# Kernel optimization log

Measured on AMD Instinct MI355X. Metric: run time of the kernel, lower is better.

Reference implementation:

```python
import jax, jax.numpy as jnp
import numpy as np

N = 50000
E = 1600000
D = 128
NUM_BOND_FEATS = 3
BOND_VOCAB = 5
BN_EPS = 1e-5


def setup_inputs() -> dict:
    key = jax.random.key(0)
    ks = jax.random.split(key, 12)
    x = jax.random.normal(ks[0], (N, D), dtype=jnp.float32)
    edge_attr = jax.random.randint(ks[1], (E, NUM_BOND_FEATS), 0, BOND_VOCAB, dtype=jnp.int64)
    src = jax.random.randint(ks[2], (E,), 0, N, dtype=jnp.int64)
    dst = jax.random.randint(ks[3], (E,), 0, N, dtype=jnp.int64)
    # BondEncoder: one embedding table per bond feature
    bond_emb = jax.random.normal(ks[4], (NUM_BOND_FEATS, BOND_VOCAB, D), dtype=jnp.float32) * 0.02
    # GIN eps parameter (init 0)
    eps = jnp.zeros((), dtype=jnp.float32)
    # MLP: Linear(D,D) -> BatchNorm1d(D) -> ReLU -> Linear(D,D)
    s = 1.0 / np.sqrt(D)
    W1 = jax.random.uniform(ks[5], (D, D), minval=-s, maxval=s, dtype=jnp.float32)
    b1 = jax.random.uniform(ks[6], (D,), minval=-s, maxval=s, dtype=jnp.float32)
    gamma = jnp.ones((D,), dtype=jnp.float32)
    beta = jnp.zeros((D,), dtype=jnp.float32)
    W2 = jax.random.uniform(ks[7], (D, D), minval=-s, maxval=s, dtype=jnp.float32)
    b2 = jax.random.uniform(ks[8], (D,), minval=-s, maxval=s, dtype=jnp.float32)
    return {"x": x, "edge_attr": edge_attr, "src": src, "dst": dst,
            "bond_emb": bond_emb, "eps": eps, "W1": W1, "b1": b1,
            "gamma": gamma, "beta": beta, "W2": W2, "b2": b2}


def reference(x, edge_attr, src, dst, bond_emb, eps, W1, b1, gamma, beta, W2, b2):
    # BondEncoder: sum of per-feature categorical embeddings -> [E, D]
    edge_embedding = bond_emb[jnp.arange(NUM_BOND_FEATS)[None, :], edge_attr].sum(axis=1)
    # copy_u gather + add edge emb + ReLU (per-edge messages)
    m = jax.nn.relu(x[src] + edge_embedding)            # [E, D]
    # scatter-sum aggregation to destination nodes
    agg = jax.ops.segment_sum(m, dst, num_segments=N)   # [N, D]
    h = (1.0 + eps) * x + agg
    # MLP: Linear -> BatchNorm (batch stats, training mode) -> ReLU -> Linear
    h1 = h @ W1 + b1
    mean = jnp.mean(h1, axis=0)
    var = jnp.var(h1, axis=0)
    hn = (h1 - mean) * jax.lax.rsqrt(var + BN_EPS) * gamma + beta
    out = jax.nn.relu(hn) @ W2 + b2
    return out
```

## Files before the change

### kernel.cpp

```cpp
#include <hip/hip_runtime.h>
#include <hip/hip_bf16.h>

#define NN 50000
#define NE 1600000
#define D 128
#define NB 196
#define CAP 9216
#define EPT 16

__device__ __forceinline__ void fma4(float4& acc, float s, const float4& w) {
  acc.x = fmaf(s, w.x, acc.x);
  acc.y = fmaf(s, w.y, acc.y);
  acc.z = fmaf(s, w.z, acc.z);
  acc.w = fmaf(s, w.w, acc.w);
}

__device__ __forceinline__ unsigned short f2bf(float f) {
  unsigned u = __float_as_uint(f);
  u += 0x7FFFu + ((u >> 16) & 1u);
  return (unsigned short)(u >> 16);
}
__device__ __forceinline__ float bf2f(unsigned short h) {
  return __uint_as_float((unsigned)h << 16);
}

__global__ __launch_bounds__(256) void k_half(const float* __restrict__ x,
                                              const float* __restrict__ bemb,
                                              ushort* __restrict__ xh,
                                              float* __restrict__ ctab) {
  const int gid = blockIdx.x * 256 + threadIdx.x;

  if (gid < 125 * D) {
    const int c = gid >> 7;
    const int k = gid & 127;
    ctab[gid] = bemb[(c / 25) * D + k] + bemb[(5 + (c % 25) / 5) * D + k] +
                bemb[(10 + c % 5) * D + k];
  }

  const int i4 = gid * 4;
  if (i4 < NN * D) {
    const float4 v = *(const float4*)(x + i4);
    ushort4 h;
    h.x = f2bf(v.x); h.y = f2bf(v.y); h.z = f2bf(v.z); h.w = f2bf(v.w);
    *(ushort4*)(xh + i4) = h;
  }
}

__global__ __launch_bounds__(256) void k_bin(const int* __restrict__ dst,
                                             const int* __restrict__ src,
                                             const int* __restrict__ ea,
                                             int* __restrict__ bucketCnt,
                                             unsigned* __restrict__ staging) {
  __shared__ int lcnt[NB], gbase[NB], lcur[NB];
  const int tid = threadIdx.x;
  for (int i = tid; i < NB; i += 256) { lcnt[i] = 0; lcur[i] = 0; }
  __syncthreads();

  const int gid = blockIdx.x * 256 + tid;
  const int e0 = gid * EPT;
  const bool act = (e0 < NE);

  int d[EPT];
  unsigned rec[EPT];
  if (act) {
    const int4* dp = (const int4*)(dst + e0);
    const int4* sp = (const int4*)(src + e0);
    const int4* ap = (const int4*)(ea + 3 * e0);
    int a[3 * EPT];
#pragma unroll
    for (int q = 0; q < (3 * EPT) / 4; ++q) {
      const int4 v = ap[q];
      a[4 * q + 0] = v.x; a[4 * q + 1] = v.y; a[4 * q + 2] = v.z; a[4 * q + 3] = v.w;
    }
#pragma unroll
    for (int q = 0; q < EPT / 4; ++q) {
      const int4 dv = dp[q];
      const int4 sv = sp[q];
      d[4 * q + 0] = dv.x; d[4 * q + 1] = dv.y; d[4 * q + 2] = dv.z; d[4 * q + 3] = dv.w;
      rec[4 * q + 0] = sv.x; rec[4 * q + 1] = sv.y; rec[4 * q + 2] = sv.z; rec[4 * q + 3] = sv.w;
    }
#pragma unroll
    for (int q = 0; q < EPT; ++q) {
      const unsigned cb = (unsigned)((a[3 * q] * 5 + a[3 * q + 1]) * 5 + a[3 * q + 2]);
      rec[q] |= (cb << 16) | ((unsigned)(d[q] & 255) << 23);
      atomicAdd(&lcnt[d[q] >> 8], 1);
    }
  }
  __syncthreads();
  for (int i = tid; i < NB; i += 256)
    gbase[i] = atomicAdd(&bucketCnt[i], lcnt[i]);
  __syncthreads();
  if (act) {
#pragma unroll
    for (int q = 0; q < EPT; ++q) {
      const int b = d[q] >> 8;
      const int r = atomicAdd(&lcur[b], 1) + gbase[b];
      if (r < CAP) staging[(size_t)b * CAP + r] = rec[q];
    }
  }
}

__global__ __launch_bounds__(256) void k_fine(const int* __restrict__ bucketCnt,
                                              const unsigned* __restrict__ staging,
                                              unsigned* __restrict__ packed2,
                                              int* __restrict__ beg,
                                              int* __restrict__ end) {
  __shared__ unsigned srec[CAP];
  __shared__ int hist[256], off[256], cur[256];
  const int tid = threadIdx.x;
  const int b = blockIdx.x;
  const int base = b * CAP;
  const int cnt = min(bucketCnt[b], CAP);

  hist[tid] = 0; cur[tid] = 0;
  for (int i = tid; i < cnt; i += 256) srec[i] = staging[base + i];
  __syncthreads();
  for (int i = tid; i < cnt; i += 256) atomicAdd(&hist[srec[i] >> 23], 1);
  __syncthreads();
  int v = hist[tid];
  off[tid] = v;
  __syncthreads();
  for (int s = 1; s < 256; s <<= 1) {
    const int u = (tid >= s) ? off[tid - s] : 0;
    __syncthreads();
    off[tid] += u;
    __syncthreads();
  }
  const int ex = off[tid] - v;
  __syncthreads();
  off[tid] = ex;
  __syncthreads();

  const int n = b * 256 + tid;
  if (n < NN) {
    beg[n] = base + off[tid];
    end[n] = base + off[tid] + hist[tid];
  }
  for (int i = tid; i < cnt; i += 256) {
    const unsigned u = srec[i];
    const int node = u >> 23;
    const int r = atomicAdd(&cur[node], 1);
    packed2[base + off[node] + r] = u & 0x7FFFFFu;
  }
}

__global__ __launch_bounds__(256, 4) void k_agg(const float* __restrict__ x,
                                                const ushort* __restrict__ xh,
                                                const float* __restrict__ ctab,
                                                const float* __restrict__ epsp,
                                                const int* __restrict__ beg,
                                                const int* __restrict__ end,
                                                const unsigned* __restrict__ packed2,
                                                float* __restrict__ hbuf) {
  const int lane = threadIdx.x & 31;
  const int n = blockIdx.x * 8 + (threadIdx.x >> 5);
  const int col = lane << 2;

  const int jb = beg[n];
  const int je = end[n];
  float4 acc = make_float4(0.f, 0.f, 0.f, 0.f);

  for (int j0 = jb; j0 < je; j0 += 32) {
    const int rem = min(32, je - j0);
    const int pk = (j0 + lane < je) ? (int)packed2[j0 + lane] : 0;
    int t = 0;
    for (; t + 8 <= rem; t += 8) {
      unsigned p[8];
#pragma unroll
      for (int i = 0; i < 8; ++i) p[i] = (unsigned)__shfl(pk, t + i, 32);
      ushort4 xs[8];
#pragma unroll
      for (int i = 0; i < 8; ++i)
        xs[i] = *(const ushort4*)(xh + (size_t)(p[i] & 0xFFFF) * D + col);
#pragma unroll
      for (int i = 0; i < 8; ++i) {
        const float4 ev = *(const float4*)(ctab + ((p[i] >> 16) & 0x7F) * D + col);
        acc.x += fmaxf(bf2f(xs[i].x) + ev.x, 0.f);
        acc.y += fmaxf(bf2f(xs[i].y) + ev.y, 0.f);
        acc.z += fmaxf(bf2f(xs[i].z) + ev.z, 0.f);
        acc.w += fmaxf(bf2f(xs[i].w) + ev.w, 0.f);
      }
    }
    for (; t < rem; ++t) {
      const unsigned p = (unsigned)__shfl(pk, t, 32);
      const ushort4 xv = *(const ushort4*)(xh + (size_t)(p & 0xFFFF) * D + col);
      const float4 ev = *(const float4*)(ctab + ((p >> 16) & 0x7F) * D + col);
      acc.x += fmaxf(bf2f(xv.x) + ev.x, 0.f);
      acc.y += fmaxf(bf2f(xv.y) + ev.y, 0.f);
      acc.z += fmaxf(bf2f(xv.z) + ev.z, 0.f);
      acc.w += fmaxf(bf2f(xv.w) + ev.w, 0.f);
    }
  }

  const float eps1 = 1.0f + epsp[0];
  const float4 xv = *(const float4*)(x + (size_t)n * D + col);
  acc.x += eps1 * xv.x;
  acc.y += eps1 * xv.y;
  acc.z += eps1 * xv.z;
  acc.w += eps1 * xv.w;
  *(float4*)(hbuf + (size_t)n * D + col) = acc;
}

__global__ __launch_bounds__(256, 2) void k_gemm1(const float* __restrict__ hbuf,
                                                  const float* __restrict__ W1,
                                                  const float* __restrict__ b1,
                                                  float* __restrict__ h1,
                                                  float* __restrict__ gsum,
                                                  float* __restrict__ gsumsq) {
  __shared__ float shT[64 * 64];
  __shared__ float sW[64 * 128];

  const int tid = threadIdx.x;
  const int row0 = blockIdx.x * 64;
  const int cg = tid & 31;
  const int rt = tid >> 5;
  const int cbase = cg * 4;
  const int rbase = rt * 8;

  float4 acc[8];
  const float4 bias = *(const float4*)(b1 + cbase);
#pragma unroll
  for (int r = 0; r < 8; ++r) acc[r] = bias;

  for (int kh = 0; kh < 2; ++kh) {
    __syncthreads();
    for (int i = tid; i < 1024; i += 256) {
      const int r = i & 63;
      const int kc = (i >> 6) << 2;
      const int gr = row0 + r;
      float4 v = make_float4(0.f, 0.f, 0.f, 0.f);
      if (gr < NN) v = *(const float4*)(hbuf + (size_t)gr * D + kh * 64 + kc);
      shT[(kc + 0) * 64 + r] = v.x;
      shT[(kc + 1) * 64 + r] = v.y;
      shT[(kc + 2) * 64 + r] = v.z;
      shT[(kc + 3) * 64 + r] = v.w;
    }
    for (int i = tid; i < 2048; i += 256) {
      const int k = i >> 5;
      const int c4 = (i & 31) << 2;
      *(float4*)(sW + k * 128 + c4) = *(const float4*)(W1 + (size_t)(kh * 64 + k) * D + c4);
    }
    __syncthreads();
    for (int k = 0; k < 64; ++k) {
      const float4 a_lo = *(const float4*)(shT + k * 64 + rbase);
      const float4 a_hi = *(const float4*)(shT + k * 64 + rbase + 4);
      const float4 w = *(const float4*)(sW + k * 128 + cbase);
      fma4(acc[0], a_lo.x, w); fma4(acc[1], a_lo.y, w);
      fma4(acc[2], a_lo.z, w); fma4(acc[3], a_lo.w, w);
      fma4(acc[4], a_hi.x, w); fma4(acc[5], a_hi.y, w);
      fma4(acc[6], a_hi.z, w); fma4(acc[7], a_hi.w, w);
    }
  }

  float4 cs = make_float4(0.f, 0.f, 0.f, 0.f);
  float4 cq = make_float4(0.f, 0.f, 0.f, 0.f);
#pragma unroll
  for (int r = 0; r < 8; ++r) {
    const int gr = row0 + rbase + r;
    if (gr < NN) {
      *(float4*)(h1 + (size_t)gr * D + cbase) = acc[r];
      cs.x += acc[r].x; cs.y += acc[r].y; cs.z += acc[r].z; cs.w += acc[r].w;
      cq.x += acc[r].x * acc[r].x; cq.y += acc[r].y * acc[r].y;
      cq.z += acc[r].z * acc[r].z; cq.w += acc[r].w * acc[r].w;
    }
  }
  __syncthreads();
  float* ssum = shT;
  float* ssq = shT + 128;
  if (tid < 128) { ssum[tid] = 0.f; ssq[tid] = 0.f; }
  __syncthreads();
  atomicAdd(&ssum[cbase + 0], cs.x);
  atomicAdd(&ssum[cbase + 1], cs.y);
  atomicAdd(&ssum[cbase + 2], cs.z);
  atomicAdd(&ssum[cbase + 3], cs.w);
  atomicAdd(&ssq[cbase + 0], cq.x);
  atomicAdd(&ssq[cbase + 1], cq.y);
  atomicAdd(&ssq[cbase + 2], cq.z);
  atomicAdd(&ssq[cbase + 3], cq.w);
  __syncthreads();
  if (tid < 128) {
    atomicAdd(&gsum[tid], ssum[tid]);
    atomicAdd(&gsumsq[tid], ssq[tid]);
  }
}

__global__ __launch_bounds__(256, 2) void k_gemm2(const float* __restrict__ hbuf,
                                                  const float* __restrict__ gsum,
                                                  const float* __restrict__ gsq,
                                                  const float* __restrict__ gamma,
                                                  const float* __restrict__ beta,
                                                  const float* __restrict__ W2,
                                                  const float* __restrict__ b2,
                                                  float* __restrict__ out) {
  __shared__ float shT[64 * 64];
  __shared__ float sW[64 * 128];

  const int tid = threadIdx.x;
  const int row0 = blockIdx.x * 64;
  const int cg = tid & 31;
  const int rt = tid >> 5;
  const int cbase = cg * 4;
  const int rbase = rt * 8;
  const float invN = 1.0f / (float)NN;

  float4 acc[8];
  const float4 bias = *(const float4*)(b2 + cbase);
#pragma unroll
  for (int r = 0; r < 8; ++r) acc[r] = bias;

  for (int kh = 0; kh < 2; ++kh) {
    __syncthreads();
    for (int i = tid; i < 1024; i += 256) {
      const int r = i & 63;
      const int kc = (i >> 6) << 2;
      const int gr = row0 + r;
      const int kk = kh * 64 + kc;
      const float4 gs = *(const float4*)(gsum + kk);
      const float4 gq = *(const float4*)(gsq + kk);
      const float4 gm = *(const float4*)(gamma + kk);
      const float4 bt = *(const float4*)(beta + kk);
      const float m0 = gs.x * invN, m1 = gs.y * invN, m2 = gs.z * invN, m3 = gs.w * invN;
      const float A0 = gm.x * rsqrtf(gq.x * invN - m0 * m0 + 1e-5f);
      const float A1 = gm.y * rsqrtf(gq.y * invN - m1 * m1 + 1e-5f);
      const float A2 = gm.z * rsqrtf(gq.z * invN - m2 * m2 + 1e-5f);
      const float A3 = gm.w * rsqrtf(gq.w * invN - m3 * m3 + 1e-5f);
      float4 v = make_float4(0.f, 0.f, 0.f, 0.f);
      if (gr < NN) {
        const float4 h = *(const float4*)(hbuf + (size_t)gr * D + kk);
        v.x = fmaxf(fmaf(h.x - m0, A0, bt.x), 0.f);
        v.y = fmaxf(fmaf(h.y - m1, A1, bt.y), 0.f);
        v.z = fmaxf(fmaf(h.z - m2, A2, bt.z), 0.f);
        v.w = fmaxf(fmaf(h.w - m3, A3, bt.w), 0.f);
      }
      shT[(kc + 0) * 64 + r] = v.x;
      shT[(kc + 1) * 64 + r] = v.y;
      shT[(kc + 2) * 64 + r] = v.z;
      shT[(kc + 3) * 64 + r] = v.w;
    }
    for (int i = tid; i < 2048; i += 256) {
      const int k = i >> 5;
      const int c4 = (i & 31) << 2;
      *(float4*)(sW + k * 128 + c4) = *(const float4*)(W2 + (size_t)(kh * 64 + k) * D + c4);
    }
    __syncthreads();
    for (int k = 0; k < 64; ++k) {
      const float4 a_lo = *(const float4*)(shT + k * 64 + rbase);
      const float4 a_hi = *(const float4*)(shT + k * 64 + rbase + 4);
      const float4 w = *(const float4*)(sW + k * 128 + cbase);
      fma4(acc[0], a_lo.x, w); fma4(acc[1], a_lo.y, w);
      fma4(acc[2], a_lo.z, w); fma4(acc[3], a_lo.w, w);
      fma4(acc[4], a_hi.x, w); fma4(acc[5], a_hi.y, w);
      fma4(acc[6], a_hi.z, w); fma4(acc[7], a_hi.w, w);
    }
  }

#pragma unroll
  for (int r = 0; r < 8; ++r) {
    const int gr = row0 + rbase + r;
    if (gr < NN) *(float4*)(out + (size_t)gr * D + cbase) = acc[r];
  }
}

extern "C" void kernel_launch(void* const* d_in, const int* in_sizes, int n_in,
                              void* d_out, int out_size, void* d_ws, size_t ws_size,
                              hipStream_t stream) {
  const float* x    = (const float*)d_in[0];
  const int* ea     = (const int*)d_in[1];
  const int* src    = (const int*)d_in[2];
  const int* dst    = (const int*)d_in[3];
  const float* bemb = (const float*)d_in[4];
  const float* epsp = (const float*)d_in[5];
  const float* W1   = (const float*)d_in[6];
  const float* b1   = (const float*)d_in[7];
  const float* gam  = (const float*)d_in[8];
  const float* bet  = (const float*)d_in[9];
  const float* W2   = (const float*)d_in[10];
  const float* b2   = (const float*)d_in[11];
  float* out = (float*)d_out;

  float* ws         = (float*)d_ws;
  float* hbuf       = ws;
  int* bucketCnt    = (int*)(ws + (size_t)NN * D);
  float* gsum       = ws + (size_t)NN * D + NB;
  float* gsumsq     = gsum + D;
  int* beg          = (int*)(gsumsq + D);
  int* endp         = beg + NN;
  float* ctab       = (float*)(endp + NN);
  ushort* xh        = (ushort*)(ctab + 125 * D);
  unsigned* staging = (unsigned*)(xh + (size_t)NN * D);
  unsigned* packed2 = staging + (size_t)NB * CAP;

  hipMemsetAsync(bucketCnt, 0, (size_t)(NB + 2 * D) * sizeof(int), stream);

  k_half<<<(NN * D / 4 + 255) / 256, 256, 0, stream>>>(x, bemb, xh, ctab);
  k_bin<<<(NE / EPT + 255) / 256, 256, 0, stream>>>(dst, src, ea, bucketCnt, staging);
  k_fine<<<NB, 256, 0, stream>>>(bucketCnt, staging, packed2, beg, endp);
  k_agg<<<NN / 8, 256, 0, stream>>>(x, xh, ctab, epsp, beg, endp, packed2, hbuf);
  k_gemm1<<<(NN + 63) / 64, 256, 0, stream>>>(hbuf, W1, b1, hbuf, gsum, gsumsq);
  k_gemm2<<<(NN + 63) / 64, 256, 0, stream>>>(hbuf, gsum, gsumsq, gam, bet, W2, b2, out);
}
```

Baseline: 319.6 us.

## Store edge-embedding table in bf16, widen agg loads, enlarge binning blocks

The combined bond embedding table is now stored as bf16, and the aggregation kernel switches to 16 lanes per node, each loading 8 columns with 16-byte loads. This halves table traffic and doubles the bytes per gather instruction. Separately, the binning and fine-sort kernels move to 1024-thread blocks, with binning doing 4 edges per thread instead of 16, and the agg occupancy hint rises to 6. Rounding the embedding table to bf16 adds some precision loss.

```diff
diff --git a/kernel.cpp b/kernel.cpp
--- a/kernel.cpp
+++ b/kernel.cpp
@@ -6,7 +6,7 @@
 #define D 128
 #define NB 196
 #define CAP 9216
-#define EPT 16
+#define EPT 4
 
 __device__ __forceinline__ void fma4(float4& acc, float s, const float4& w) {
   acc.x = fmaf(s, w.x, acc.x);
@@ -20,21 +20,33 @@
   u += 0x7FFFu + ((u >> 16) & 1u);
   return (unsigned short)(u >> 16);
 }
-__device__ __forceinline__ float bf2f(unsigned short h) {
-  return __uint_as_float((unsigned)h << 16);
+
+__device__ __forceinline__ void acc8(float* acc, const uint4& xv, const uint4& ev) {
+  const unsigned xx[4] = {xv.x, xv.y, xv.z, xv.w};
+  const unsigned ee[4] = {ev.x, ev.y, ev.z, ev.w};
+#pragma unroll
+  for (int q = 0; q < 4; ++q) {
+    const float xl = __uint_as_float(xx[q] << 16);
+    const float xh_ = __uint_as_float(xx[q] & 0xFFFF0000u);
+    const float el = __uint_as_float(ee[q] << 16);
+    const float eh = __uint_as_float(ee[q] & 0xFFFF0000u);
+    acc[2 * q + 0] += fmaxf(xl + el, 0.f);
+    acc[2 * q + 1] += fmaxf(xh_ + eh, 0.f);
+  }
 }
 
 __global__ __launch_bounds__(256) void k_half(const float* __restrict__ x,
                                               const float* __restrict__ bemb,
                                               ushort* __restrict__ xh,
-                                              float* __restrict__ ctab) {
+                                              ushort* __restrict__ cth) {
   const int gid = blockIdx.x * 256 + threadIdx.x;
 
   if (gid < 125 * D) {
     const int c = gid >> 7;
     const int k = gid & 127;
-    ctab[gid] = bemb[(c / 25) * D + k] + bemb[(5 + (c % 25) / 5) * D + k] +
-                bemb[(10 + c % 5) * D + k];
+    const float v = bemb[(c / 25) * D + k] + bemb[(5 + (c % 25) / 5) * D + k] +
+                    bemb[(10 + c % 5) * D + k];
+    cth[gid] = f2bf(v);
   }
 
   const int i4 = gid * 4;
@@ -46,39 +58,34 @@
   }
 }
 
-__global__ __launch_bounds__(256) void k_bin(const int* __restrict__ dst,
-                                             const int* __restrict__ src,
-                                             const int* __restrict__ ea,
-                                             int* __restrict__ bucketCnt,
-                                             unsigned* __restrict__ staging) {
+__global__ __launch_bounds__(1024) void k_bin(const int* __restrict__ dst,
+                                              const int* __restrict__ src,
+                                              const int* __restrict__ ea,
+                                              int* __restrict__ bucketCnt,
+                                              unsigned* __restrict__ staging) {
   __shared__ int lcnt[NB], gbase[NB], lcur[NB];
   const int tid = threadIdx.x;
-  for (int i = tid; i < NB; i += 256) { lcnt[i] = 0; lcur[i] = 0; }
-  __syncthreads();
-
-  const int gid = blockIdx.x * 256 + tid;
+  for (int i = tid; i < NB; i += 1024) { lcnt[i] = 0; lcur[i] = 0; }
+  __syncthreads();
+
+  const int gid = blockIdx.x * 1024 + tid;
   const int e0 = gid * EPT;
   const bool act = (e0 < NE);
 
   int d[EPT];
   unsigned rec[EPT];
   if (act) {
-    const int4* dp = (const int4*)(dst + e0);
-    const int4* sp = (const int4*)(src + e0);
+    const int4 dv = *(const int4*)(dst + e0);
+    const int4 sv = *(const int4*)(src + e0);
     const int4* ap = (const int4*)(ea + 3 * e0);
-    int a[3 * EPT];
-#pragma unroll
-    for (int q = 0; q < (3 * EPT) / 4; ++q) {
+    int a[12];
+#pragma unroll
+    for (int q = 0; q < 3; ++q) {
       const int4 v = ap[q];
       a[4 * q + 0] = v.x; a[4 * q + 1] = v.y; a[4 * q + 2] = v.z; a[4 * q + 3] = v.w;
     }
-#pragma unroll
-    for (int q = 0; q < EPT / 4; ++q) {
-      const int4 dv = dp[q];
-      const int4 sv = sp[q];
-      d[4 * q + 0] = dv.x; d[4 * q + 1] = dv.y; d[4 * q + 2] = dv.z; d[4 * q + 3] = dv.w;
-      rec[4 * q + 0] = sv.x; rec[4 * q + 1] = sv.y; rec[4 * q + 2] = sv.z; rec[4 * q + 3] = sv.w;
-    }
+    d[0] = dv.x; d[1] = dv.y; d[2] = dv.z; d[3] = dv.w;
+    rec[0] = sv.x; rec[1] = sv.y; rec[2] = sv.z; rec[3] = sv.w;
 #pragma unroll
     for (int q = 0; q < EPT; ++q) {
       const unsigned cb = (unsigned)((a[3 * q] * 5 + a[3 * q + 1]) * 5 + a[3 * q + 2]);
@@ -87,7 +94,7 @@
     }
   }
   __syncthreads();
-  for (int i = tid; i < NB; i += 256)
+  for (int i = tid; i < NB; i += 1024)
     gbase[i] = atomicAdd(&bucketCnt[i], lcnt[i]);
   __syncthreads();
   if (act) {
@@ -100,11 +107,11 @@
   }
 }
 
-__global__ __launch_bounds__(256) void k_fine(const int* __restrict__ bucketCnt,
-                                              const unsigned* __restrict__ staging,
-                                              unsigned* __restrict__ packed2,
-                                              int* __restrict__ beg,
-                                              int* __restrict__ end) {
+__global__ __launch_bounds__(1024) void k_fine(const int* __restrict__ bucketCnt,
+                                               const unsigned* __restrict__ staging,
+                                               unsigned* __restrict__ packed2,
+                                               int* __restrict__ beg,
+                                               int* __restrict__ end) {
   __shared__ unsigned srec[CAP];
   __shared__ int hist[256], off[256], cur[256];
   const int tid = threadIdx.x;
@@ -112,31 +119,32 @@
   const int base = b * CAP;
   const int cnt = min(bucketCnt[b], CAP);
 
-  hist[tid] = 0; cur[tid] = 0;
-  for (int i = tid; i < cnt; i += 256) srec[i] = staging[base + i];
-  __syncthreads();
-  for (int i = tid; i < cnt; i += 256) atomicAdd(&hist[srec[i] >> 23], 1);
-  __syncthreads();
-  int v = hist[tid];
-  off[tid] = v;
+  if (tid < 256) { hist[tid] = 0; cur[tid] = 0; }
+  for (int i = tid; i < cnt; i += 1024) srec[i] = staging[base + i];
+  __syncthreads();
+  for (int i = tid; i < cnt; i += 1024) atomicAdd(&hist[srec[i] >> 23], 1);
+  __syncthreads();
+  int v = 0;
+  if (tid < 256) { v = hist[tid]; off[tid] = v; }
   __syncthreads();
   for (int s = 1; s < 256; s <<= 1) {
-    const int u = (tid >= s) ? off[tid - s] : 0;
-    __syncthreads();
-    off[tid] += u;
-    __syncthreads();
-  }
-  const int ex = off[tid] - v;
-  __syncthreads();
-  off[tid] = ex;
-  __syncthreads();
-
-  const int n = b * 256 + tid;
-  if (n < NN) {
-    beg[n] = base + off[tid];
-    end[n] = base + off[tid] + hist[tid];
-  }
-  for (int i = tid; i < cnt; i += 256) {
+    int u = 0;
+    if (tid < 256 && tid >= s) u = off[tid - s];
+    __syncthreads();
+    if (tid < 256) off[tid] += u;
+    __syncthreads();
+  }
+  if (tid < 256) off[tid] -= v;
+  __syncthreads();
+
+  if (tid < 256) {
+    const int n = b * 256 + tid;
+    if (n < NN) {
+      beg[n] = base + off[tid];
+      end[n] = base + off[tid] + hist[tid];
+    }
+  }
+  for (int i = tid; i < cnt; i += 1024) {
     const unsigned u = srec[i];
     const int node = u >> 23;
     const int r = atomicAdd(&cur[node], 1);
@@ -144,61 +152,59 @@
   }
 }
 
-__global__ __launch_bounds__(256, 4) void k_agg(const float* __restrict__ x,
+__global__ __launch_bounds__(256, 6) void k_agg(const float* __restrict__ x,
                                                 const ushort* __restrict__ xh,
-                                                const float* __restrict__ ctab,
+                                                const ushort* __restrict__ cth,
                                                 const float* __restrict__ epsp,
                                                 const int* __restrict__ beg,
                                                 const int* __restrict__ end,
                                                 const unsigned* __restrict__ packed2,
                                                 float* __restrict__ hbuf) {
-  const int lane = threadIdx.x & 31;
-  const int n = blockIdx.x * 8 + (threadIdx.x >> 5);
-  const int col = lane << 2;
+  const int lane = threadIdx.x & 15;
+  const int n = blockIdx.x * 16 + (threadIdx.x >> 4);
+  const int col = lane << 3;
 
   const int jb = beg[n];
   const int je = end[n];
-  float4 acc = make_float4(0.f, 0.f, 0.f, 0.f);
-
-  for (int j0 = jb; j0 < je; j0 += 32) {
-    const int rem = min(32, je - j0);
+  float acc[8] = {0.f, 0.f, 0.f, 0.f, 0.f, 0.f, 0.f, 0.f};
+
+  for (int j0 = jb; j0 < je; j0 += 16) {
+    const int rem = min(16, je - j0);
     const int pk = (j0 + lane < je) ? (int)packed2[j0 + lane] : 0;
     int t = 0;
     for (; t + 8 <= rem; t += 8) {
       unsigned p[8];
 #pragma unroll
-      for (int i = 0; i < 8; ++i) p[i] = (unsigned)__shfl(pk, t + i, 32);
-      ushort4 xs[8];
+      for (int i = 0; i < 8; ++i) p[i] = (unsigned)__shfl(pk, t + i, 16);
+      uint4 xs[8];
 #pragma unroll
       for (int i = 0; i < 8; ++i)
-        xs[i] = *(const ushort4*)(xh + (size_t)(p[i] & 0xFFFF) * D + col);
+        xs[i] = *(const uint4*)(xh + (size_t)(p[i] & 0xFFFF) * D + col);
 #pragma unroll
       for (int i = 0; i < 8; ++i) {
-        const float4 ev = *(const float4*)(ctab + ((p[i] >> 16) & 0x7F) * D + col);
-        acc.x += fmaxf(bf2f(xs[i].x) + ev.x, 0.f);
-        acc.y += fmaxf(bf2f(xs[i].y) + ev.y, 0.f);
-        acc.z += fmaxf(bf2f(xs[i].z) + ev.z, 0.f);
-        acc.w += fmaxf(bf2f(xs[i].w) + ev.w, 0.f);
+        const uint4 ev = *(const uint4*)(cth + ((p[i] >> 16) & 0x7F) * D + col);
+        acc8(acc, xs[i], ev);
       }
     }
     for (; t < rem; ++t) {
-      const unsigned p = (unsigned)__shfl(pk, t, 32);
-      const ushort4 xv = *(const ushort4*)(xh + (size_t)(p & 0xFFFF) * D + col);
-      const float4 ev = *(const float4*)(ctab + ((p >> 16) & 0x7F) * D + col);
-      acc.x += fmaxf(bf2f(xv.x) + ev.x, 0.f);
-      acc.y += fmaxf(bf2f(xv.y) + ev.y, 0.f);
-      acc.z += fmaxf(bf2f(xv.z) + ev.z, 0.f);
-      acc.w += fmaxf(bf2f(xv.w) + ev.w, 0.f);
+      const unsigned p = (unsigned)__shfl(pk, t, 16);
+      const uint4 xv = *(const uint4*)(xh + (size_t)(p & 0xFFFF) * D + col);
+      const uint4 ev = *(const uint4*)(cth + ((p >> 16) & 0x7F) * D + col);
+      acc8(acc, xv, ev);
     }
   }
 
   const float eps1 = 1.0f + epsp[0];
-  const float4 xv = *(const float4*)(x + (size_t)n * D + col);
-  acc.x += eps1 * xv.x;
-  acc.y += eps1 * xv.y;
-  acc.z += eps1 * xv.z;
-  acc.w += eps1 * xv.w;
-  *(float4*)(hbuf + (size_t)n * D + col) = acc;
+  const float4 xa = *(const float4*)(x + (size_t)n * D + col);
+  const float4 xb = *(const float4*)(x + (size_t)n * D + col + 4);
+  acc[0] += eps1 * xa.x; acc[1] += eps1 * xa.y;
+  acc[2] += eps1 * xa.z; acc[3] += eps1 * xa.w;
+  acc[4] += eps1 * xb.x; acc[5] += eps1 * xb.y;
+  acc[6] += eps1 * xb.z; acc[7] += eps1 * xb.w;
+  float4 o0 = make_float4(acc[0], acc[1], acc[2], acc[3]);
+  float4 o1 = make_float4(acc[4], acc[5], acc[6], acc[7]);
+  *(float4*)(hbuf + (size_t)n * D + col) = o0;
+  *(float4*)(hbuf + (size_t)n * D + col + 4) = o1;
 }
 
 __global__ __launch_bounds__(256, 2) void k_gemm1(const float* __restrict__ hbuf,
@@ -385,17 +391,17 @@
   float* gsumsq     = gsum + D;
   int* beg          = (int*)(gsumsq + D);
   int* endp         = beg + NN;
-  float* ctab       = (float*)(endp + NN);
-  ushort* xh        = (ushort*)(ctab + 125 * D);
+  ushort* cth       = (ushort*)(endp + NN);
+  ushort* xh        = cth + 125 * D;
   unsigned* staging = (unsigned*)(xh + (size_t)NN * D);
   unsigned* packed2 = staging + (size_t)NB * CAP;
 
   hipMemsetAsync(bucketCnt, 0, (size_t)(NB + 2 * D) * sizeof(int), stream);
 
-  k_half<<<(NN * D / 4 + 255) / 256, 256, 0, stream>>>(x, bemb, xh, ctab);
-  k_bin<<<(NE / EPT + 255) / 256, 256, 0, stream>>>(dst, src, ea, bucketCnt, staging);
-  k_fine<<<NB, 256, 0, stream>>>(bucketCnt, staging, packed2, beg, endp);
-  k_agg<<<NN / 8, 256, 0, stream>>>(x, xh, ctab, epsp, beg, endp, packed2, hbuf);
+  k_half<<<(NN * D / 4 + 255) / 256, 256, 0, stream>>>(x, bemb, xh, cth);
+  k_bin<<<(NE / EPT + 1023) / 1024, 1024, 0, stream>>>(dst, src, ea, bucketCnt, staging);
+  k_fine<<<NB, 1024, 0, stream>>>(bucketCnt, staging, packed2, beg, endp);
+  k_agg<<<NN / 16, 256, 0, stream>>>(x, xh, cth, epsp, beg, endp, packed2, hbuf);
   k_gemm1<<<(NN + 63) / 64, 256, 0, stream>>>(hbuf, W1, b1, hbuf, gsum, gsumsq);
   k_gemm2<<<(NN + 63) / 64, 256, 0, stream>>>(hbuf, gsum, gsumsq, gam, bet, W2, b2, out);
 }
```

New measurement: 347.0 us. +8.6%, slower.
